# Optimization experiments

Measured on AMD Instinct MI355X. Metric: run time of the kernel, lower is better.

## Reference

```python
import jax, jax.numpy as jnp
import numpy as np

B, T, C, HS = 4, 2048, 1024, 64

def setup_inputs() -> dict:
    key = jax.random.key(0)
    k1, k2, k3, k4 = jax.random.split(key, 4)
    x = jax.random.normal(k1, (B, T, C), dtype=jnp.float32)
    # torch Linear default init scale ~ 1/sqrt(fan_in); scale weights similarly
    s = C ** -0.5
    Wq = jax.random.normal(k2, (C, HS), dtype=jnp.float32) * s
    Wk = jax.random.normal(k3, (C, HS), dtype=jnp.float32) * s
    Wv = jax.random.normal(k4, (C, HS), dtype=jnp.float32) * s
    return {"x": x, "Wq": Wq, "Wk": Wk, "Wv": Wv}

def reference(x, Wq, Wk, Wv):
    B_, T_, C_ = x.shape
    q = x @ Wq          # [B,T,HS]
    k = x @ Wk          # [B,T,HS]
    v = x @ Wv          # [B,T,HS]
    scale = C_ ** -0.5  # note: module scales by input dim C, not head_size
    w = jnp.einsum('bqh,bkh->bqk', q, k) * scale  # [B,T,T]
    causal = jnp.tril(jnp.ones((T_, T_), dtype=bool))
    w = jnp.where(causal, w, -jnp.inf)
    a = jax.nn.softmax(w, axis=-1)  # dropout is identity (eval / drop_rate=0)
    return jnp.einsum('bqk,bkh->bqh', a, v)
```

## Files before the change

kernel.cpp:

```cpp
#include <hip/hip_runtime.h>
#include <math.h>

#define B_  4
#define T_  2048
#define C_  1024
#define HS_ 64
#define M_  (B_*T_)
#define NCAT 192
#define SCALE_ 0.03125f

typedef unsigned short ushort_t;
typedef short bf16x8 __attribute__((ext_vector_type(8)));
typedef float f32x4 __attribute__((ext_vector_type(4)));

static __device__ __forceinline__ unsigned short f2bf(float f) {
    union { float f; unsigned int u; } c; c.f = f;
    unsigned int u = c.u;
    return (unsigned short)((u + 0x7FFFu + ((u >> 16) & 1u)) >> 16);
}
static __device__ __forceinline__ unsigned short f2bf_fast(float f) {
    union { float f; unsigned int u; } c; c.f = f;
    return (unsigned short)((c.u + 0x8000u) >> 16);
}
static __device__ __forceinline__ float b2f(unsigned short u) {
    union { unsigned int u; float f; } c; c.u = ((unsigned int)u) << 16;
    return c.f;
}

__global__ void wconv_kernel(const float* __restrict__ Wq, const float* __restrict__ Wk,
                             const float* __restrict__ Wv, ushort_t* __restrict__ wt) {
    int idx = (blockIdx.x * 256 + threadIdx.x) * 4;
    int n = idx >> 10;
    int k0 = idx & 1023;
    const float* W = (n < 64) ? Wq : (n < 128) ? Wk : Wv;
    int nn = n & 63;
    ushort_t o0 = f2bf(W[(k0 + 0) * HS_ + nn]);
    ushort_t o1 = f2bf(W[(k0 + 1) * HS_ + nn]);
    ushort_t o2 = f2bf(W[(k0 + 2) * HS_ + nn]);
    ushort_t o3 = f2bf(W[(k0 + 3) * HS_ + nn]);
    uint2 d;
    d.x = (unsigned)o0 | ((unsigned)o1 << 16);
    d.y = (unsigned)o2 | ((unsigned)o3 << 16);
    *(uint2*)(wt + (size_t)n * C_ + k0) = d;
}

__global__ __launch_bounds__(512, 4) void proj_kernel(const float* __restrict__ x,
    const ushort_t* __restrict__ wt,
    ushort_t* __restrict__ qws, ushort_t* __restrict__ kws, ushort_t* __restrict__ vt) {
    __shared__ __align__(16) f32x4 red[4][12 * 64];

    int tid  = threadIdx.x;
    int wid  = tid >> 6;
    int lane = tid & 63;
    int qd   = lane >> 4;
    int lq   = lane & 15;
    int r0   = blockIdx.x * 16;

    f32x4 acc[12];
    #pragma unroll
    for (int i = 0; i < 12; i++) acc[i] = (f32x4){0.f,0.f,0.f,0.f};

    const float*    xp = x  + (size_t)(r0 + lq) * C_ + wid * 128 + qd * 8;
    const ushort_t* wp = wt + (size_t)lq * C_ + wid * 128 + qd * 8;

    #pragma unroll
    for (int i = 0; i < 4; i++) {
        float4 a0 = *(const float4*)(xp + i * 32);
        float4 a1 = *(const float4*)(xp + i * 32 + 4);
        union { bf16x8 v; ushort_t u[8]; } af;
        af.u[0] = f2bf(a0.x); af.u[1] = f2bf(a0.y); af.u[2] = f2bf(a0.z); af.u[3] = f2bf(a0.w);
        af.u[4] = f2bf(a1.x); af.u[5] = f2bf(a1.y); af.u[6] = f2bf(a1.z); af.u[7] = f2bf(a1.w);
        #pragma unroll
        for (int nt = 0; nt < 12; nt++) {
            bf16x8 bv = *(const bf16x8*)(wp + (size_t)nt * 16 * C_ + i * 32);
            acc[nt] = __builtin_amdgcn_mfma_f32_16x16x32_bf16(af.v, bv, acc[nt], 0, 0, 0);
        }
    }

    if (wid >= 4) {
        #pragma unroll
        for (int nt = 0; nt < 12; nt++) red[wid - 4][nt * 64 + lane] = acc[nt];
    }
    __syncthreads();
    if (wid < 4) {
        #pragma unroll
        for (int nt = 0; nt < 12; nt++) acc[nt] += red[wid][nt * 64 + lane];
    }
    __syncthreads();
    if (wid == 2 || wid == 3) {
        #pragma unroll
        for (int nt = 0; nt < 12; nt++) red[wid][nt * 64 + lane] = acc[nt];
    }
    __syncthreads();
    if (wid < 2) {
        #pragma unroll
        for (int nt = 0; nt < 12; nt++) acc[nt] += red[wid + 2][nt * 64 + lane];
    }
    __syncthreads();
    if (wid == 1) {
        #pragma unroll
        for (int nt = 0; nt < 12; nt++) red[0][nt * 64 + lane] = acc[nt];
    }
    __syncthreads();
    if (wid == 0) {
        #pragma unroll
        for (int nt = 0; nt < 12; nt++) {
            acc[nt] += red[0][nt * 64 + lane];
            int outn = nt >> 2;
            int col  = (nt & 3) * 16 + lq;
            #pragma unroll
            for (int r = 0; r < 4; r++) {
                int row = r0 + qd * 4 + r;
                float v = acc[nt][r];
                if (outn == 0) v *= SCALE_;
                ushort_t val = f2bf(v);
                if (outn == 0)      qws[(size_t)row * HS_ + col] = val;
                else if (outn == 1) kws[(size_t)row * HS_ + col] = val;
                else {
                    int b = row >> 11, t = row & 2047;
                    vt[((size_t)b * 64 + col) * T_ + t] = val;
                }
            }
        }
    }
}

__global__ __launch_bounds__(128) void flash_kernel(const ushort_t* __restrict__ qws,
    const ushort_t* __restrict__ kws, const ushort_t* __restrict__ vt,
    ushort_t* __restrict__ opart, float* __restrict__ lpart) {
    __shared__ __align__(16) ushort_t Pw[2][16 * 72];

    int tid  = threadIdx.x;
    int wid  = tid >> 6;
    int lane = tid & 63;
    int qd   = lane >> 4;
    int lq   = lane & 15;

    int batch = blockIdx.y;
    int idx   = blockIdx.x;
    int g = (int)((sqrtf(2.f * idx + 1.f) - 1.f) * 0.5f);
    while (2 * (g + 1) * (g + 2) <= idx) g++;
    while (2 * g * (g + 1) > idx) g--;
    int rem  = idx - 2 * g * (g + 1);
    int tile = 4 * g + rem / (g + 1);
    int c    = rem % (g + 1);

    int q0   = tile * 32;
    int qrow = q0 + wid * 16 + lq;
    int grow = batch * T_ + qrow;

    bf16x8 qf[2];
    #pragma unroll
    for (int st = 0; st < 2; st++)
        qf[st] = *(const bf16x8*)(qws + (size_t)grow * HS_ + st * 32 + qd * 8);

    float lsum = 0.f;
    f32x4 O[4];
    #pragma unroll
    for (int nt = 0; nt < 4; nt++) O[nt] = (f32x4){0.f,0.f,0.f,0.f};

    int kstart = c * 128;
    int klimit = q0 + 32;
    int kend   = (kstart + 128 < klimit) ? kstart + 128 : klimit;

    ushort_t* pw = &Pw[wid][lq * 72];
    const ushort_t* kp = kws + (size_t)batch * T_ * HS_;
    const ushort_t* vbase = vt + (size_t)batch * 64 * T_;

    for (int kb = kstart; kb < kend; kb += 64) {
        bf16x8 kf[8], vf[8];
        #pragma unroll
        for (int sub = 0; sub < 4; sub++)
            #pragma unroll
            for (int st = 0; st < 2; st++)
                kf[sub * 2 + st] = *(const bf16x8*)(kp + (size_t)(kb + sub * 16 + lq) * HS_ + st * 32 + qd * 8);
        #pragma unroll
        for (int nt = 0; nt < 4; nt++)
            #pragma unroll
            for (int kk = 0; kk < 2; kk++)
                vf[nt * 2 + kk] = *(const bf16x8*)(vbase + ((size_t)nt * 16 + lq) * T_ + kb + kk * 32 + qd * 8);

        f32x4 S[4];
        #pragma unroll
        for (int sub = 0; sub < 4; sub++) {
            f32x4 s = (f32x4){0.f,0.f,0.f,0.f};
            #pragma unroll
            for (int st = 0; st < 2; st++)
                s = __builtin_amdgcn_mfma_f32_16x16x32_bf16(kf[sub * 2 + st], qf[st], s, 0, 0, 0);
            S[sub] = s;
        }

        if (kb + 64 > q0) {
            #pragma unroll
            for (int sub = 0; sub < 4; sub++)
                #pragma unroll
                for (int r = 0; r < 4; r++) {
                    int key = kb + sub * 16 + qd * 4 + r;
                    float p = (key <= qrow) ? __expf(S[sub][r]) : 0.f;
                    S[sub][r] = p;
                    lsum += p;
                }
        } else {
            #pragma unroll
            for (int sub = 0; sub < 4; sub++)
                #pragma unroll
                for (int r = 0; r < 4; r++) {
                    float p = __expf(S[sub][r]);
                    S[sub][r] = p;
                    lsum += p;
                }
        }

        #pragma unroll
        for (int sub = 0; sub < 4; sub++) {
            uint2 d;
            d.x = (unsigned)f2bf_fast(S[sub][0]) | ((unsigned)f2bf_fast(S[sub][1]) << 16);
            d.y = (unsigned)f2bf_fast(S[sub][2]) | ((unsigned)f2bf_fast(S[sub][3]) << 16);
            *(uint2*)(pw + sub * 16 + qd * 4) = d;
        }
        bf16x8 pf0 = *(const bf16x8*)(pw + qd * 8);
        bf16x8 pf1 = *(const bf16x8*)(pw + 32 + qd * 8);

        #pragma unroll
        for (int nt = 0; nt < 4; nt++) {
            O[nt] = __builtin_amdgcn_mfma_f32_16x16x32_bf16(vf[nt * 2 + 0], pf0, O[nt], 0, 0, 0);
            O[nt] = __builtin_amdgcn_mfma_f32_16x16x32_bf16(vf[nt * 2 + 1], pf1, O[nt], 0, 0, 0);
        }
    }

    lsum += __shfl_xor(lsum, 16, 64);
    lsum += __shfl_xor(lsum, 32, 64);

    #pragma unroll
    for (int nt = 0; nt < 4; nt++) {
        uint2 d;
        d.x = (unsigned)f2bf_fast(O[nt][0]) | ((unsigned)f2bf_fast(O[nt][1]) << 16);
        d.y = (unsigned)f2bf_fast(O[nt][2]) | ((unsigned)f2bf_fast(O[nt][3]) << 16);
        *(uint2*)(opart + ((size_t)c * M_ + grow) * HS_ + nt * 16 + qd * 4) = d;
    }
    if (qd == 0) lpart[(size_t)c * M_ + grow] = lsum;
}

__global__ void combine_kernel(const ushort_t* __restrict__ opart,
    const float* __restrict__ lpart, float* __restrict__ out) {
    int idx = blockIdx.x * 256 + threadIdx.x;
    int row = idx >> 4;
    int d   = (idx & 15) << 2;
    int nc  = ((row & 2047) >> 7) + 1;

    float L = 0.f;
    float4 acc = make_float4(0.f, 0.f, 0.f, 0.f);
    for (int c = 0; c < nc; c++) {
        L += lpart[(size_t)c * M_ + row];
        const ushort_t* op = opart + ((size_t)c * M_ + row) * HS_ + d;
        ushort2 a = *(const ushort2*)op;
        ushort2 b = *(const ushort2*)(op + 2);
        acc.x += b2f(a.x); acc.y += b2f(a.y);
        acc.z += b2f(b.x); acc.w += b2f(b.y);
    }
    float li = 1.f / L;
    *(float4*)(out + (size_t)row * HS_ + d) =
        make_float4(acc.x * li, acc.y * li, acc.z * li, acc.w * li);
}

extern "C" void kernel_launch(void* const* d_in, const int* in_sizes, int n_in,
                              void* d_out, int out_size, void* d_ws, size_t ws_size,
                              hipStream_t stream) {
    const float* x  = (const float*)d_in[0];
    const float* Wq = (const float*)d_in[1];
    const float* Wk = (const float*)d_in[2];
    const float* Wv = (const float*)d_in[3];
    float* out = (float*)d_out;

    ushort_t* wt  = (ushort_t*)d_ws;
    ushort_t* qws = wt  + (size_t)NCAT * C_;
    ushort_t* kws = qws + (size_t)M_ * HS_;
    ushort_t* vt  = kws + (size_t)M_ * HS_;
    float* lpart  = (float*)(vt + (size_t)M_ * HS_);
    ushort_t* opart = (ushort_t*)(lpart + (size_t)16 * M_);

    wconv_kernel<<<NCAT * C_ / (256 * 4), 256, 0, stream>>>(Wq, Wk, Wv, wt);
    proj_kernel<<<512, 512, 0, stream>>>(x, wt, qws, kws, vt);
    flash_kernel<<<dim3(544, 4), 128, 0, stream>>>(qws, kws, vt, opart, lpart);
    combine_kernel<<<M_ * 16 / 256, 256, 0, stream>>>(opart, lpart, out);
}
```

Before: 132.5 us.

## Fuse split-K combine into flash kernel via in-block wave reduction

Drops the global opart/lpart partial buffers and the separate combine kernel. Each 1024-thread block now handles two 16-row query tiles (p and 127-p) to balance causal work. Eight waves split the key range per tile, and their partial O and row sums are merged by an LDS tree reduction before the normalised fp32 output is written directly. This removes a launch and the partial-sum traffic through global memory. In exchange, each K/V load serves only 16 query rows, there are several block-wide barriers, and the grid is just one large block per CU.

```diff
diff --git a/kernel.cpp b/kernel.cpp
--- a/kernel.cpp
+++ b/kernel.cpp
@@ -21,10 +21,6 @@
 static __device__ __forceinline__ unsigned short f2bf_fast(float f) {
     union { float f; unsigned int u; } c; c.f = f;
     return (unsigned short)((c.u + 0x8000u) >> 16);
-}
-static __device__ __forceinline__ float b2f(unsigned short u) {
-    union { unsigned int u; float f; } c; c.u = ((unsigned int)u) << 16;
-    return c.f;
 }
 
 __global__ void wconv_kernel(const float* __restrict__ Wq, const float* __restrict__ Wk,
@@ -125,29 +121,26 @@
     }
 }
 
-__global__ __launch_bounds__(128) void flash_kernel(const ushort_t* __restrict__ qws,
+__global__ __launch_bounds__(1024) void flash_kernel(const ushort_t* __restrict__ qws,
     const ushort_t* __restrict__ kws, const ushort_t* __restrict__ vt,
-    ushort_t* __restrict__ opart, float* __restrict__ lpart) {
-    __shared__ __align__(16) ushort_t Pw[2][16 * 72];
+    float* __restrict__ out) {
+    __shared__ __align__(16) unsigned char pool[36864];
 
     int tid  = threadIdx.x;
     int wid  = tid >> 6;
     int lane = tid & 63;
     int qd   = lane >> 4;
     int lq   = lane & 15;
+    int ts   = wid >> 3;
+    int ws   = wid & 7;
 
     int batch = blockIdx.y;
-    int idx   = blockIdx.x;
-    int g = (int)((sqrtf(2.f * idx + 1.f) - 1.f) * 0.5f);
-    while (2 * (g + 1) * (g + 2) <= idx) g++;
-    while (2 * g * (g + 1) > idx) g--;
-    int rem  = idx - 2 * g * (g + 1);
-    int tile = 4 * g + rem / (g + 1);
-    int c    = rem % (g + 1);
-
-    int q0   = tile * 32;
-    int qrow = q0 + wid * 16 + lq;
-    int grow = batch * T_ + qrow;
+    int p     = blockIdx.x;
+    int tile  = ts ? (127 - p) : p;
+    int q0    = tile * 16;
+    int qrow  = q0 + lq;
+    int grow  = batch * T_ + qrow;
+    int nU    = (q0 + 16 + 63) >> 6;
 
     bf16x8 qf[2];
     #pragma unroll
@@ -159,26 +152,19 @@
     #pragma unroll
     for (int nt = 0; nt < 4; nt++) O[nt] = (f32x4){0.f,0.f,0.f,0.f};
 
-    int kstart = c * 128;
-    int klimit = q0 + 32;
-    int kend   = (kstart + 128 < klimit) ? kstart + 128 : klimit;
-
-    ushort_t* pw = &Pw[wid][lq * 72];
-    const ushort_t* kp = kws + (size_t)batch * T_ * HS_;
-    const ushort_t* vbase = vt + (size_t)batch * 64 * T_;
-
-    for (int kb = kstart; kb < kend; kb += 64) {
-        bf16x8 kf[8], vf[8];
+    ushort_t* pw = (ushort_t*)pool + wid * 1152 + lq * 72;
+    const ushort_t* kp    = kws + (size_t)batch * T_ * HS_;
+    const ushort_t* vbase = vt  + (size_t)batch * 64 * T_;
+
+    for (int u = ws; u < nU; u += 8) {
+        int kb = u * 64;
+
+        bf16x8 kf[8];
         #pragma unroll
         for (int sub = 0; sub < 4; sub++)
             #pragma unroll
             for (int st = 0; st < 2; st++)
                 kf[sub * 2 + st] = *(const bf16x8*)(kp + (size_t)(kb + sub * 16 + lq) * HS_ + st * 32 + qd * 8);
-        #pragma unroll
-        for (int nt = 0; nt < 4; nt++)
-            #pragma unroll
-            for (int kk = 0; kk < 2; kk++)
-                vf[nt * 2 + kk] = *(const bf16x8*)(vbase + ((size_t)nt * 16 + lq) * T_ + kb + kk * 32 + qd * 8);
 
         f32x4 S[4];
         #pragma unroll
@@ -189,6 +175,13 @@
                 s = __builtin_amdgcn_mfma_f32_16x16x32_bf16(kf[sub * 2 + st], qf[st], s, 0, 0, 0);
             S[sub] = s;
         }
+
+        bf16x8 vf[8];
+        #pragma unroll
+        for (int nt = 0; nt < 4; nt++)
+            #pragma unroll
+            for (int kk = 0; kk < 2; kk++)
+                vf[nt * 2 + kk] = *(const bf16x8*)(vbase + ((size_t)nt * 16 + lq) * T_ + kb + kk * 32 + qd * 8);
 
         if (kb + 64 > q0) {
             #pragma unroll
@@ -196,18 +189,18 @@
                 #pragma unroll
                 for (int r = 0; r < 4; r++) {
                     int key = kb + sub * 16 + qd * 4 + r;
-                    float p = (key <= qrow) ? __expf(S[sub][r]) : 0.f;
-                    S[sub][r] = p;
-                    lsum += p;
+                    float pv = (key <= qrow) ? __expf(S[sub][r]) : 0.f;
+                    S[sub][r] = pv;
+                    lsum += pv;
                 }
         } else {
             #pragma unroll
             for (int sub = 0; sub < 4; sub++)
                 #pragma unroll
                 for (int r = 0; r < 4; r++) {
-                    float p = __expf(S[sub][r]);
-                    S[sub][r] = p;
-                    lsum += p;
+                    float pv = __expf(S[sub][r]);
+                    S[sub][r] = pv;
+                    lsum += pv;
                 }
         }
 
@@ -228,39 +221,64 @@
         }
     }
 
-    lsum += __shfl_xor(lsum, 16, 64);
-    lsum += __shfl_xor(lsum, 32, 64);
-
-    #pragma unroll
-    for (int nt = 0; nt < 4; nt++) {
-        uint2 d;
-        d.x = (unsigned)f2bf_fast(O[nt][0]) | ((unsigned)f2bf_fast(O[nt][1]) << 16);
-        d.y = (unsigned)f2bf_fast(O[nt][2]) | ((unsigned)f2bf_fast(O[nt][3]) << 16);
-        *(uint2*)(opart + ((size_t)c * M_ + grow) * HS_ + nt * 16 + qd * 4) = d;
-    }
-    if (qd == 0) lpart[(size_t)c * M_ + grow] = lsum;
-}
-
-__global__ void combine_kernel(const ushort_t* __restrict__ opart,
-    const float* __restrict__ lpart, float* __restrict__ out) {
-    int idx = blockIdx.x * 256 + threadIdx.x;
-    int row = idx >> 4;
-    int d   = (idx & 15) << 2;
-    int nc  = ((row & 2047) >> 7) + 1;
-
-    float L = 0.f;
-    float4 acc = make_float4(0.f, 0.f, 0.f, 0.f);
-    for (int c = 0; c < nc; c++) {
-        L += lpart[(size_t)c * M_ + row];
-        const ushort_t* op = opart + ((size_t)c * M_ + row) * HS_ + d;
-        ushort2 a = *(const ushort2*)op;
-        ushort2 b = *(const ushort2*)(op + 2);
-        acc.x += b2f(a.x); acc.y += b2f(a.y);
-        acc.z += b2f(b.x); acc.w += b2f(b.y);
-    }
-    float li = 1.f / L;
-    *(float4*)(out + (size_t)row * HS_ + d) =
-        make_float4(acc.x * li, acc.y * li, acc.z * li, acc.w * li);
+    f32x4* red  = (f32x4*)pool;
+    float* lred = (float*)(pool + 32768);
+    __syncthreads();
+    if (ws >= 4) {
+        int sl = ts * 4 + (ws - 4);
+        f32x4* rs = red + (size_t)sl * 256;
+        #pragma unroll
+        for (int nt = 0; nt < 4; nt++) rs[nt * 64 + lane] = O[nt];
+        lred[sl * 64 + lane] = lsum;
+    }
+    __syncthreads();
+    if (ws < 4) {
+        int sl = ts * 4 + ws;
+        f32x4* rs = red + (size_t)sl * 256;
+        #pragma unroll
+        for (int nt = 0; nt < 4; nt++) O[nt] += rs[nt * 64 + lane];
+        lsum += lred[sl * 64 + lane];
+    }
+    __syncthreads();
+    if (ws == 2 || ws == 3) {
+        int sl = ts * 4 + (ws - 2);
+        f32x4* rs = red + (size_t)sl * 256;
+        #pragma unroll
+        for (int nt = 0; nt < 4; nt++) rs[nt * 64 + lane] = O[nt];
+        lred[sl * 64 + lane] = lsum;
+    }
+    __syncthreads();
+    if (ws < 2) {
+        int sl = ts * 4 + ws;
+        f32x4* rs = red + (size_t)sl * 256;
+        #pragma unroll
+        for (int nt = 0; nt < 4; nt++) O[nt] += rs[nt * 64 + lane];
+        lsum += lred[sl * 64 + lane];
+    }
+    __syncthreads();
+    if (ws == 1) {
+        int sl = ts * 4;
+        f32x4* rs = red + (size_t)sl * 256;
+        #pragma unroll
+        for (int nt = 0; nt < 4; nt++) rs[nt * 64 + lane] = O[nt];
+        lred[sl * 64 + lane] = lsum;
+    }
+    __syncthreads();
+    if (ws == 0) {
+        int sl = ts * 4;
+        f32x4* rs = red + (size_t)sl * 256;
+        #pragma unroll
+        for (int nt = 0; nt < 4; nt++) O[nt] += rs[nt * 64 + lane];
+        lsum += lred[sl * 64 + lane];
+        lsum += __shfl_xor(lsum, 16, 64);
+        lsum += __shfl_xor(lsum, 32, 64);
+        float li = 1.f / lsum;
+        #pragma unroll
+        for (int nt = 0; nt < 4; nt++) {
+            f32x4 o = O[nt] * li;
+            *(f32x4*)(out + (size_t)grow * HS_ + nt * 16 + qd * 4) = o;
+        }
+    }
 }
 
 extern "C" void kernel_launch(void* const* d_in, const int* in_sizes, int n_in,
@@ -276,11 +294,8 @@
     ushort_t* qws = wt  + (size_t)NCAT * C_;
     ushort_t* kws = qws + (size_t)M_ * HS_;
     ushort_t* vt  = kws + (size_t)M_ * HS_;
-    float* lpart  = (float*)(vt + (size_t)M_ * HS_);
-    ushort_t* opart = (ushort_t*)(lpart + (size_t)16 * M_);
 
     wconv_kernel<<<NCAT * C_ / (256 * 4), 256, 0, stream>>>(Wq, Wk, Wv, wt);
     proj_kernel<<<512, 512, 0, stream>>>(x, wt, qws, kws, vt);
-    flash_kernel<<<dim3(544, 4), 128, 0, stream>>>(qws, kws, vt, opart, lpart);
-    combine_kernel<<<M_ * 16 / 256, 256, 0, stream>>>(opart, lpart, out);
-}
+    flash_kernel<<<dim3(64, 4), 1024, 0, stream>>>(qws, kws, vt, out);
+}
```

Result: faster. 122.2 us (-7.8%).
